# Optimization experiments

Hardware: AMD Instinct MI355X
Metric: run time of the kernel (lower is better)

## Reference

```python
import jax, jax.numpy as jnp
import numpy as np

B, ENC_T, ENC_D = 16, 600, 512
H = 512          # hidden_size == attn_dim (Attention built with attn_dim=hidden_size)
A = 512
VOCAB = 8000
MAX_LEN = 64
SOS = 1


def setup_inputs() -> dict:
    key = jax.random.key(0)
    ks = jax.random.split(key, 16)
    n = jax.random.normal
    s = 0.04  # param init scale
    return {
        "encoder_outputs": n(ks[0], (B, ENC_T, ENC_D), dtype=jnp.float32),
        # embedding table
        "emb": n(ks[1], (VOCAB, H)) * 0.05,
        # GRU (1 layer, input = hidden + enc_dim), PyTorch layout [3H, in]/[3H, H]
        "w_ih": n(ks[2], (3 * H, H + ENC_D)) * s,
        "w_hh": n(ks[3], (3 * H, H)) * s,
        "b_ih": n(ks[4], (3 * H,)) * s,
        "b_hh": n(ks[5], (3 * H,)) * s,
        # location attention: Conv1d(1 -> A, k=3, pad=1)
        "conv_w": n(ks[6], (A, 1, 3)) * 0.1,
        "conv_b": n(ks[7], (A,)) * 0.1,
        "attn_W": n(ks[8], (A, H)) * s,      # W: dec_dim -> attn_dim, no bias
        "attn_V": n(ks[9], (A, ENC_D)) * s,  # V: enc_dim -> attn_dim, no bias
        "attn_fc_w": n(ks[10], (1, A)) * s,  # fc: attn_dim -> 1, with bias
        "attn_fc_b": n(ks[11], (1,)) * s,
        "attn_b": n(ks[12], (A,)) * s,       # extra learned bias b
        # output projection: (hidden + enc_dim) -> vocab
        "fc_w": n(ks[13], (VOCAB, H + ENC_D)) * s,
        "fc_b": n(ks[14], (VOCAB,)) * s,
    }


def reference(encoder_outputs, emb, w_ih, w_hh, b_ih, b_hh,
              conv_w, conv_b, attn_W, attn_V, attn_fc_w, attn_fc_b, attn_b,
              fc_w, fc_b):
    dt = encoder_outputs.dtype
    b, t, ed = encoder_outputs.shape
    h_dim = emb.shape[1]

    # V(values) is time-invariant across decode steps: precompute once. [B, T, A]
    Vv = jnp.einsum('btd,ad->bta', encoder_outputs, attn_V)

    tok0 = jnp.full((b,), SOS, dtype=jnp.int32)
    h0 = jnp.zeros((b, h_dim), dt)          # GRU hidden (None -> zeros)
    ctx0 = jnp.zeros((b, ed), dt)           # initial context
    aw0 = jnp.zeros((b, t), dt)             # initial attention weights

    def step(carry, _):
        tok, h, ctx, aw = carry
        # embed + concat with previous context  [B, H+E]
        x = jnp.concatenate([emb[tok], ctx], axis=-1)
        # GRU cell (PyTorch gate order r, z, n)
        gx = x @ w_ih.T + b_ih
        gh = h @ w_hh.T + b_hh
        xr, xz, xn = jnp.split(gx, 3, axis=-1)
        hr, hz, hn = jnp.split(gh, 3, axis=-1)
        r = jax.nn.sigmoid(xr + hr)
        z = jax.nn.sigmoid(xz + hz)
        ncand = jnp.tanh(xn + r * hn)
        h_new = (1.0 - z) * ncand + z * h
        # location feature: Conv1d over last attention weights. [B, A, T] -> [B, T, A]
        conv = jax.lax.conv_general_dilated(
            aw[:, None, :], conv_w, window_strides=(1,), padding=[(1, 1)],
            dimension_numbers=('NCH', 'OIH', 'NCH')) + conv_b[None, :, None]
        conv = jnp.transpose(conv, (0, 2, 1))
        # score = fc(tanh(W(q) + V(values) + conv + b))  [B, T]
        wq = h_new @ attn_W.T                      # [B, A]
        e = jnp.tanh(wq[:, None, :] + Vv + conv + attn_b)
        score = jnp.einsum('bta,a->bt', e, attn_fc_w[0]) + attn_fc_b[0]
        aw_new = jax.nn.softmax(score, axis=-1)
        # context = attn_weight @ values  [B, E]
        ctx_new = jnp.einsum('bt,btd->bd', aw_new, encoder_outputs)
        # output projection + log_softmax
        out = jnp.concatenate([h_new, ctx_new], axis=-1)
        logits = out @ fc_w.T + fc_b
        logp = jax.nn.log_softmax(logits, axis=-1)
        tok_new = jnp.argmax(logp, axis=-1).astype(jnp.int32)  # greedy symbol
        return (tok_new, h_new, ctx_new, aw_new), logp

    _, logps = jax.lax.scan(step, (tok0, h0, ctx0, aw0), None, length=MAX_LEN)
    # [T_dec, B, V] -> [B, T_dec, V], matching stacked decoder_outputs
    return jnp.transpose(logps, (1, 0, 2))
```

## Files before the change

kernel.cpp:

```cpp
#include <hip/hip_runtime.h>
#include <math.h>

#define NG 256
#define NT 512
#define XSS 516
#define NLOGW 250

__device__ __forceinline__ float ldc(const float* p) {
    return __hip_atomic_load(p, __ATOMIC_RELAXED, __HIP_MEMORY_SCOPE_AGENT);
}
__device__ __forceinline__ void stc(float* p, float v) {
    __hip_atomic_store(p, v, __ATOMIC_RELAXED, __HIP_MEMORY_SCOPE_AGENT);
}

__device__ __forceinline__ void gbar(int* flags, int e, int g, int tid) {
    __syncthreads();
    if (tid == 0)
        __hip_atomic_store(flags + g * 32, e, __ATOMIC_RELAXED,
                           __HIP_MEMORY_SCOPE_AGENT);
    if (tid < 64) {
        const int l = tid;
        int miss = 0;
        for (;;) {
            int f0 = __hip_atomic_load(flags + l * 32,         __ATOMIC_RELAXED, __HIP_MEMORY_SCOPE_AGENT);
            int f1 = __hip_atomic_load(flags + (64 + l) * 32,  __ATOMIC_RELAXED, __HIP_MEMORY_SCOPE_AGENT);
            int f2 = __hip_atomic_load(flags + (128 + l) * 32, __ATOMIC_RELAXED, __HIP_MEMORY_SCOPE_AGENT);
            int f3 = __hip_atomic_load(flags + (192 + l) * 32, __ATOMIC_RELAXED, __HIP_MEMORY_SCOPE_AGENT);
            int m = min(min(f0, f1), min(f2, f3));
            if (__all(m >= e)) break;
            if (++miss > 2) __builtin_amdgcn_s_sleep(1);
        }
    }
    __syncthreads();
}

__global__ __launch_bounds__(256) void k_vv(const float* __restrict__ enc,
                                            const float* __restrict__ attn_V,
                                            float* __restrict__ Vv) {
    int wg = blockIdx.x;
    int b = wg / 40, t0 = (wg % 40) * 15;
    int tid = threadIdx.x;
    __shared__ __align__(16) float encL[15][512];
    for (int i = tid; i < 15 * 512; i += 256) {
        int tl = i >> 9, d = i & 511;
        encL[tl][d] = enc[((size_t)(b * 600) + (t0 + tl)) * 512 + d];
    }
    __syncthreads();
    for (int half = 0; half < 2; ++half) {
        int a = tid + half * 256;
        const float4* wrow = reinterpret_cast<const float4*>(attn_V + (size_t)a * 512);
        float acc[15];
#pragma unroll
        for (int tl = 0; tl < 15; ++tl) acc[tl] = 0.f;
        for (int k = 0; k < 128; ++k) {
            float4 w = wrow[k];
#pragma unroll
            for (int tl = 0; tl < 15; ++tl) {
                float4 x = reinterpret_cast<const float4*>(&encL[tl][0])[k];
                acc[tl] += w.x * x.x + w.y * x.y + w.z * x.z + w.w * x.w;
            }
        }
        for (int tl = 0; tl < 15; ++tl)
            Vv[((size_t)(b * 600) + (t0 + tl)) * 512 + a] = acc[tl];
    }
}

__global__ __launch_bounds__(NT, 1) void mega(
    const float* __restrict__ enc, const float* __restrict__ emb,
    const float* __restrict__ w_ih, const float* __restrict__ w_hh,
    const float* __restrict__ b_ih, const float* __restrict__ b_hh,
    const float* __restrict__ conv_w, const float* __restrict__ conv_b,
    const float* __restrict__ attn_W, const float* __restrict__ attn_fc_w,
    const float* __restrict__ attn_fc_b, const float* __restrict__ attn_b,
    const float* __restrict__ fc_w, const float* __restrict__ fc_b,
    const float* __restrict__ Vv,
    float* hbuf, float* ctxg, float* awg, float* scoreg, float* wqg,
    float* part, float* logZ, int* cnt, float* dout)
{
    const int g = blockIdx.x;
    const int tid = threadIdx.x;
    const int bg = g & 15;
    int bs = 0;

    __shared__ float xs[16 * XSS];
    __shared__ float aux[2600];

    for (int s = 0; s < 64; ++s) {
        const int p = s & 1;
        {
            float* pg = aux;
            float* tokf = aux + 2048;
            if (s == 0) {
                if (tid < 16) tokf[tid] = 1.0f;
                __syncthreads();
            } else {
                const int wv = tid >> 6, lane = tid & 63;
                for (int b = wv; b < 16; b += 8) {
                    float M = -3.4e38f, S = 0.f, I = 0.f;
                    for (int q = 0; q < 4; ++q) {
                        int pw = lane + (q << 6);
                        if (pw < NLOGW) {
                            const float* r = part + ((size_t)pw * 16 + b) * 4;
                            float m = ldc(r), se2 = ldc(r + 1), ii = ldc(r + 2);
                            if (m > M)      { S = S * expf(M - m) + se2; M = m; I = ii; }
                            else if (m == M){ S += se2; if (ii < I) I = ii; }
                            else            { S += se2 * expf(m - M); }
                        }
                    }
                    for (int off = 32; off; off >>= 1) {
                        float m  = __shfl_xor(M, off, 64);
                        float se2 = __shfl_xor(S, off, 64);
                        float ii = __shfl_xor(I, off, 64);
                        if (m > M)      { S = S * expf(M - m) + se2; M = m; I = ii; }
                        else if (m == M){ S += se2; if (ii < I) I = ii; }
                        else            { S += se2 * expf(m - M); }
                    }
                    if (lane == 0) {
                        tokf[b] = I;
                        if (g == 0) stc(&logZ[(s - 1) * 16 + b], M + logf(S));
                    }
                }
                __syncthreads();
            }
            const int b  = tid & 15;
            const int u  = tid >> 4;
            const int il = u & 1;
            const int pr = u >> 1;
            const int i  = (g << 1) + il;
            float ar = 0.f, az = 0.f, axn = 0.f, ahn = 0.f;
            for (int pass = 0; pass < 3; ++pass) {
                for (int idx = tid; idx < 8192; idx += NT) {
                    int bb = idx >> 9, k = idx & 511;
                    float v;
                    if (pass == 0)      v = emb[(size_t)((int)tokf[bb]) * 512 + k];
                    else if (pass == 1) v = ldc(&ctxg[(bb << 9) + k]);
                    else                v = ldc(&hbuf[((p << 4) + bb) * 512 + k]);
                    xs[bb * XSS + k] = v;
                }
                __syncthreads();
                const float* wbase = (pass == 2) ? w_hh : w_ih;
                const size_t rl = (pass == 2) ? 512 : 1024;
                const int ko = (pass == 1) ? 512 : 0;
                const float4* wr = (const float4*)(wbase + (size_t)i * rl + ko) + (pr << 3);
                const float4* wz = (const float4*)(wbase + (size_t)(512 + i) * rl + ko) + (pr << 3);
                const float4* wn = (const float4*)(wbase + (size_t)(1024 + i) * rl + ko) + (pr << 3);
                const float4* xv = (const float4*)(xs + b * XSS) + (pr << 3);
                float s0 = 0.f, s1 = 0.f, s2 = 0.f;
#pragma unroll
                for (int k = 0; k < 8; ++k) {
                    float4 x = xv[k];
                    float4 a = wr[k]; s0 += a.x*x.x + a.y*x.y + a.z*x.z + a.w*x.w;
                    float4 c = wz[k]; s1 += c.x*x.x + c.y*x.y + c.z*x.z + c.w*x.w;
                    float4 d = wn[k]; s2 += d.x*x.x + d.y*x.y + d.z*x.z + d.w*x.w;
                }
                ar += s0; az += s1;
                if (pass < 2) axn += s2; else ahn += s2;
                if (pass < 2) __syncthreads();
            }
            {
                int base = (((b << 1) + il) << 4) + pr;
                pg[base] = ar; pg[512 + base] = az;
                pg[1024 + base] = axn; pg[1536 + base] = ahn;
            }
            __syncthreads();
            if (tid < 32) {
                int bb = tid & 15, ill = tid >> 4;
                int ii = (g << 1) + ill;
                float sr = 0.f, sz2 = 0.f, sxn = 0.f, shn = 0.f;
                int bs2 = ((bb << 1) + ill) << 4;
                for (int q = 0; q < 16; ++q) {
                    sr  += pg[bs2 + q];        sz2 += pg[512 + bs2 + q];
                    sxn += pg[1024 + bs2 + q]; shn += pg[1536 + bs2 + q];
                }
                sr  += b_ih[ii] + b_hh[ii];
                sz2 += b_ih[512 + ii] + b_hh[512 + ii];
                sxn += b_ih[1024 + ii];
                shn += b_hh[1024 + ii];
                float r = 1.f / (1.f + expf(-sr));
                float z = 1.f / (1.f + expf(-sz2));
                float n = tanhf(sxn + r * shn);
                float hp = xs[bb * XSS + ii];
                stc(&hbuf[(((p ^ 1) << 4) + bb) * 512 + ii], (1.f - z) * n + z * hp);
            }
        }
        gbar(cnt, ++bs, g, tid);

        {
            const int ac = g >> 4;
            for (int idx = tid; idx < 512; idx += NT)
                xs[idx] = ldc(&hbuf[(((p ^ 1) << 4) + bg) * 512 + idx]);
            __syncthreads();
            const int al = tid >> 4, ln = tid & 15;
            const int a = (ac << 5) + al;
            const float4* wr = (const float4*)(attn_W + (size_t)a * 512) + (ln << 3);
            const float4* hv = (const float4*)xs + (ln << 3);
            float acc = 0.f;
#pragma unroll
            for (int k = 0; k < 8; ++k) {
                float4 w = wr[k], x = hv[k];
                acc += w.x*x.x + w.y*x.y + w.z*x.z + w.w*x.w;
            }
            for (int off = 8; off; off >>= 1) acc += __shfl_xor(acc, off, 64);
            if (ln == 0) stc(&wqg[(bg << 9) + a], acc);
        }
        gbar(cnt, ++bs, g, tid);

        {
            const int tc = g >> 4;
            const int t0 = tc * 38;
            float* wqL  = xs;
            float* cw0  = xs + 512;
            float* cw1  = xs + 1024;
            float* cw2  = xs + 1536;
            float* cbab = xs + 2048;
            float* fcwL = xs + 2560;
            for (int a = tid; a < 512; a += NT) {
                wqL[a]  = ldc(&wqg[(bg << 9) + a]);
                cw0[a]  = conv_w[a * 3];
                cw1[a]  = conv_w[a * 3 + 1];
                cw2[a]  = conv_w[a * 3 + 2];
                cbab[a] = conv_b[a] + attn_b[a];
                fcwL[a] = attn_fc_w[a];
            }
            __syncthreads();
            const float fcb = attn_fc_b[0];
            const int wv = tid >> 6, lane = tid & 63;
            for (int tl = wv; tl < 38; tl += 8) {
                const int t = t0 + tl;
                if (t < 600) {
                    const float awm = (t > 0)   ? ldc(&awg[bg * 600 + t - 1]) : 0.f;
                    const float aw0 = ldc(&awg[bg * 600 + t]);
                    const float awp = (t < 599) ? ldc(&awg[bg * 600 + t + 1]) : 0.f;
                    const float* vv = Vv + ((size_t)bg * 600 + t) * 512;
                    float acc = 0.f;
#pragma unroll
                    for (int q = 0; q < 8; ++q) {
                        const int a = lane + (q << 6);
                        float uu = wqL[a] + vv[a] + cbab[a]
                                 + cw0[a] * awm + cw1[a] * aw0 + cw2[a] * awp;
                        acc += tanhf(uu) * fcwL[a];
                    }
                    for (int off = 32; off; off >>= 1) acc += __shfl_xor(acc, off, 64);
                    if (lane == 0) stc(&scoreg[bg * 600 + t], acc + fcb);
                }
            }
        }
        gbar(cnt, ++bs, g, tid);

        {
            const int ec = g >> 4;
            float* pb    = xs;
            float* wredM = aux + 2064;
            float* wredS = aux + 2080;
            float* red16 = aux;
            float lm = -3.4e38f;
            for (int t = tid; t < 600; t += NT) {
                float v = ldc(&scoreg[bg * 600 + t]);
                pb[t] = v;
                lm = fmaxf(lm, v);
            }
            for (int off = 32; off; off >>= 1) lm = fmaxf(lm, __shfl_xor(lm, off, 64));
            if ((tid & 63) == 0) wredM[tid >> 6] = lm;
            __syncthreads();
            float M = wredM[0];
#pragma unroll
            for (int q = 1; q < 8; ++q) M = fmaxf(M, wredM[q]);
            float lsum = 0.f;
            for (int t = tid; t < 600; t += NT) {
                float e = expf(pb[t] - M);
                pb[t] = e;
                lsum += e;
            }
            for (int off = 32; off; off >>= 1) lsum += __shfl_xor(lsum, off, 64);
            if ((tid & 63) == 0) wredS[tid >> 6] = lsum;
            __syncthreads();
            float S = 0.f;
#pragma unroll
            for (int q = 0; q < 8; ++q) S += wredS[q];
            const float invS = 1.f / S;
            if (ec == 0)
                for (int t = tid; t < 600; t += NT) stc(&awg[bg * 600 + t], pb[t] * invS);
            const int tg = tid >> 5, l32 = tid & 31;
            const int e = (ec << 5) + l32;
            float acc = 0.f;
            for (int t = tg; t < 600; t += 16)
                acc += pb[t] * enc[((size_t)bg * 600 + t) * 512 + e];
            red16[(tg << 5) + l32] = acc;
            __syncthreads();
            if (tg == 0) {
                float a2 = 0.f;
#pragma unroll
                for (int q = 0; q < 16; ++q) a2 += red16[(q << 5) + l32];
                stc(&ctxg[(bg << 9) + e], a2 * invS);
            }
        }
        gbar(cnt, ++bs, g, tid);

        {
            float* accL = aux;
            float acc0 = 0.f, acc1 = 0.f;
            const int bb = tid & 15, jj = (tid >> 4) & 15;
            const int act = (tid < 256);
            const int v0 = (g << 5) + (jj << 1);
            for (int pass = 0; pass < 2; ++pass) {
                for (int idx = tid; idx < 8192; idx += NT) {
                    int b2 = idx >> 9, k = idx & 511;
                    xs[b2 * XSS + k] = pass ? ldc(&ctxg[(b2 << 9) + k])
                                            : ldc(&hbuf[(((p ^ 1) << 4) + b2) * 512 + k]);
                }
                __syncthreads();
                if (g < NLOGW && act) {
                    const float4* w0 = (const float4*)(fc_w + (size_t)v0 * 1024 + (pass << 9));
                    const float4* w1 = (const float4*)(fc_w + (size_t)(v0 + 1) * 1024 + (pass << 9));
                    const float4* xv = (const float4*)(xs + bb * XSS);
#pragma unroll 4
                    for (int k = 0; k < 128; ++k) {
                        float4 x = xv[k];
                        float4 a = w0[k]; acc0 += a.x*x.x + a.y*x.y + a.z*x.z + a.w*x.w;
                        float4 c = w1[k]; acc1 += c.x*x.x + c.y*x.y + c.z*x.z + c.w*x.w;
                    }
                }
                __syncthreads();
            }
            if (g < NLOGW && act) {
                acc0 += fc_b[v0]; acc1 += fc_b[v0 + 1];
                float* o = dout + ((size_t)bb * 64 + s) * 8000;
                stc(o + v0, acc0);
                stc(o + v0 + 1, acc1);
                float bv, bi;
                if (acc0 >= acc1) { bv = acc0; bi = (float)v0; }
                else              { bv = acc1; bi = (float)(v0 + 1); }
                float se2 = expf(acc0 - bv) + expf(acc1 - bv);
                int rbase = (((bb << 4) + jj) << 2);
                accL[rbase] = bv; accL[rbase + 1] = bi; accL[rbase + 2] = se2;
            }
            __syncthreads();
            if (g < NLOGW && tid < 16) {
                float M = -3.4e38f, I = 0.f, S = 0.f;
                for (int q = 0; q < 16; ++q) {
                    int rb = (((tid << 4) + q) << 2);
                    float m = accL[rb], ii = accL[rb + 1], se2 = accL[rb + 2];
                    if (m > M)      { S = S * expf(M - m) + se2; M = m; I = ii; }
                    else if (m == M){ S += se2; if (ii < I) I = ii; }
                    else            { S += se2 * expf(m - M); }
                }
                float* pr2 = part + ((size_t)g * 16 + tid) * 4;
                stc(pr2, M); stc(pr2 + 1, S); stc(pr2 + 2, I);
            }
        }
        gbar(cnt, ++bs, g, tid);
    }

    if (g == 0) {
        const int wv = tid >> 6, lane = tid & 63;
        for (int b = wv; b < 16; b += 8) {
            float M = -3.4e38f, S = 0.f;
            for (int q = 0; q < 4; ++q) {
                int pw = lane + (q << 6);
                if (pw < NLOGW) {
                    const float* r = part + ((size_t)pw * 16 + b) * 4;
                    float m = ldc(r), se2 = ldc(r + 1);
                    if (m > M)      { S = S * expf(M - m) + se2; M = m; }
                    else if (m == M){ S += se2; }
                    else            { S += se2 * expf(m - M); }
                }
            }
            for (int off = 32; off; off >>= 1) {
                float m  = __shfl_xor(M, off, 64);
                float se2 = __shfl_xor(S, off, 64);
                if (m > M)      { S = S * expf(M - m) + se2; M = m; }
                else if (m == M){ S += se2; }
                else            { S += se2 * expf(m - M); }
            }
            if (lane == 0) stc(&logZ[63 * 16 + b], M + logf(S));
        }
    }
    gbar(cnt, ++bs, g, tid);
    for (int r = g; r < 1024; r += NG) {
        float z = ldc(&logZ[(r & 63) * 16 + (r >> 6)]);
        float* o = dout + (size_t)r * 8000;
        for (int i = tid; i < 8000; i += NT) o[i] -= z;
    }
}

extern "C" void kernel_launch(void* const* d_in, const int* in_sizes, int n_in,
                              void* d_out, int out_size, void* d_ws, size_t ws_size,
                              hipStream_t stream) {
    const float* enc       = (const float*)d_in[0];
    const float* emb       = (const float*)d_in[1];
    const float* w_ih      = (const float*)d_in[2];
    const float* w_hh      = (const float*)d_in[3];
    const float* b_ih      = (const float*)d_in[4];
    const float* b_hh      = (const float*)d_in[5];
    const float* conv_w    = (const float*)d_in[6];
    const float* conv_b    = (const float*)d_in[7];
    const float* attn_W    = (const float*)d_in[8];
    const float* attn_V    = (const float*)d_in[9];
    const float* attn_fc_w = (const float*)d_in[10];
    const float* attn_fc_b = (const float*)d_in[11];
    const float* attn_b    = (const float*)d_in[12];
    const float* fc_w      = (const float*)d_in[13];
    const float* fc_b      = (const float*)d_in[14];

    float* ws    = (float*)d_ws;
    float* Vv    = ws;
    float* hbuf  = Vv + 4915200;
    float* ctx   = hbuf + 16384;
    float* aw    = ctx + 8192;
    float* score = aw + 9600;
    float* wq    = score + 9600;
    float* part  = wq + 8192;
    float* logZ  = part + 16384;
    int*   cnt   = (int*)(logZ + 1024);
    float* dout  = (float*)d_out;

    hipMemsetAsync(hbuf, 0, 34176 * sizeof(float), stream);
    hipMemsetAsync(cnt, 0, 8192 * sizeof(int), stream);

    k_vv<<<dim3(640), dim3(256), 0, stream>>>(enc, attn_V, Vv);

    void* args[] = {(void*)&enc, (void*)&emb, (void*)&w_ih, (void*)&w_hh,
                    (void*)&b_ih, (void*)&b_hh, (void*)&conv_w, (void*)&conv_b,
                    (void*)&attn_W, (void*)&attn_fc_w, (void*)&attn_fc_b,
                    (void*)&attn_b, (void*)&fc_w, (void*)&fc_b, (void*)&Vv,
                    (void*)&hbuf, (void*)&ctx, (void*)&aw, (void*)&score,
                    (void*)&wq, (void*)&part, (void*)&logZ, (void*)&cnt,
                    (void*)&dout};
    hipLaunchCooperativeKernel(reinterpret_cast<void*>(mega),
                               dim3(NG), dim3(NT), args, 0, stream);
}
```

Baseline: 7.034 ms.

## Use per-step buffers, hierarchical atomic barrier, plain vector loads, and restructured logits GEMV

Replaces the flag-polling grid barrier with a two-level atomic counter barrier where a single thread per block spins on a go flag. Each decode step now writes its own fresh buffers for h, ctx, wq, score, aw and partials instead of double-buffering. Because no location is ever rewritten, cross-block reads can use plain vectorized float4 loads rather than relaxed atomic loads. The output projection is reorganized so one thread computes one vocab row per batch with a wave-level argmax/logsumexp merge. Encoder and Vv streams are loaded nontemporally. The cost is a larger workspace, and correctness now relies on the release/acquire behaviour of relaxed atomics plus non-coherent caches seeing each step's fresh addresses.

Result: slower. 8.532 ms (+21.3%).

```diff
diff --git a/kernel.cpp b/kernel.cpp
--- a/kernel.cpp
+++ b/kernel.cpp
@@ -3,35 +3,41 @@
 
 #define NG 256
 #define NT 512
-#define XSS 516
+#define XS2 1032
 #define NLOGW 250
 
-__device__ __forceinline__ float ldc(const float* p) {
-    return __hip_atomic_load(p, __ATOMIC_RELAXED, __HIP_MEMORY_SCOPE_AGENT);
-}
 __device__ __forceinline__ void stc(float* p, float v) {
     __hip_atomic_store(p, v, __ATOMIC_RELAXED, __HIP_MEMORY_SCOPE_AGENT);
 }
 
-__device__ __forceinline__ void gbar(int* flags, int e, int g, int tid) {
+__device__ __forceinline__ void gbar(int* cnt, int epoch, int g, int tid) {
     __syncthreads();
-    if (tid == 0)
-        __hip_atomic_store(flags + g * 32, e, __ATOMIC_RELAXED,
-                           __HIP_MEMORY_SCOPE_AGENT);
-    if (tid < 64) {
-        const int l = tid;
-        int miss = 0;
-        for (;;) {
-            int f0 = __hip_atomic_load(flags + l * 32,         __ATOMIC_RELAXED, __HIP_MEMORY_SCOPE_AGENT);
-            int f1 = __hip_atomic_load(flags + (64 + l) * 32,  __ATOMIC_RELAXED, __HIP_MEMORY_SCOPE_AGENT);
-            int f2 = __hip_atomic_load(flags + (128 + l) * 32, __ATOMIC_RELAXED, __HIP_MEMORY_SCOPE_AGENT);
-            int f3 = __hip_atomic_load(flags + (192 + l) * 32, __ATOMIC_RELAXED, __HIP_MEMORY_SCOPE_AGENT);
-            int m = min(min(f0, f1), min(f2, f3));
-            if (__all(m >= e)) break;
-            if (++miss > 2) __builtin_amdgcn_s_sleep(1);
-        }
+    if (tid == 0) {
+        int* c0 = cnt + ((g & 15) << 5);
+        int* c1 = cnt + 512;
+        int* go = cnt + 576;
+        int r = __hip_atomic_fetch_add(c0, 1, __ATOMIC_RELAXED,
+                                       __HIP_MEMORY_SCOPE_AGENT);
+        if (r == (epoch << 4) - 1) {
+            int r2 = __hip_atomic_fetch_add(c1, 1, __ATOMIC_RELAXED,
+                                            __HIP_MEMORY_SCOPE_AGENT);
+            if (r2 == (epoch << 4) - 1)
+                __hip_atomic_store(go, epoch, __ATOMIC_RELAXED,
+                                   __HIP_MEMORY_SCOPE_AGENT);
+        }
+        int it = 0;
+        while (__hip_atomic_load(go, __ATOMIC_RELAXED,
+                                 __HIP_MEMORY_SCOPE_AGENT) < epoch)
+            if (++it > 4) __builtin_amdgcn_s_sleep(8);
     }
     __syncthreads();
+}
+
+__device__ __forceinline__ void merge3(float& M, float& S, float& I,
+                                       float m, float se, float ii) {
+    if (m > M)       { S = S * expf(M - m) + se; M = m; I = ii; }
+    else if (m == M) { S += se; if (ii < I) I = ii; }
+    else             { S += se * expf(m - M); }
 }
 
 __global__ __launch_bounds__(256) void k_vv(const float* __restrict__ enc,
@@ -73,20 +79,29 @@
     const float* __restrict__ attn_W, const float* __restrict__ attn_fc_w,
     const float* __restrict__ attn_fc_b, const float* __restrict__ attn_b,
     const float* __restrict__ fc_w, const float* __restrict__ fc_b,
-    const float* __restrict__ Vv,
-    float* hbuf, float* ctxg, float* awg, float* scoreg, float* wqg,
-    float* part, float* logZ, int* cnt, float* dout)
+    const float* __restrict__ Vv, const float* __restrict__ Z,
+    float* hv, float* cv, float* wqv, float* scv, float* awv, float* pav,
+    float* logZ, int* cnt, float* dout)
 {
     const int g = blockIdx.x;
     const int tid = threadIdx.x;
     const int bg = g & 15;
-    int bs = 0;
-
-    __shared__ float xs[16 * XSS];
+    int ep = 0;
+
+    __shared__ __align__(16) float xs[16 * XS2];
     __shared__ float aux[2600];
 
     for (int s = 0; s < 64; ++s) {
-        const int p = s & 1;
+        const float* h_r   = (s == 0) ? Z         : hv + (size_t)(s - 1) * 8192;
+        const float* ctx_r = (s == 0) ? Z + 8192  : cv + (size_t)(s - 1) * 8192;
+        const float* aw_r  = (s == 0) ? Z + 16384 : awv + (size_t)(s - 1) * 9600;
+        float* h_w   = hv  + (size_t)s * 8192;
+        float* ctx_w = cv  + (size_t)s * 8192;
+        float* aw_w  = awv + (size_t)s * 9600;
+        float* wq_s  = wqv + (size_t)s * 8192;
+        float* sc_s  = scv + (size_t)s * 9600;
+        float* pa_w  = pav + (size_t)s * 16384;
+
         {
             float* pg = aux;
             float* tokf = aux + 2048;
@@ -94,27 +109,20 @@
                 if (tid < 16) tokf[tid] = 1.0f;
                 __syncthreads();
             } else {
+                const float* pa_r = pav + (size_t)(s - 1) * 16384;
                 const int wv = tid >> 6, lane = tid & 63;
                 for (int b = wv; b < 16; b += 8) {
                     float M = -3.4e38f, S = 0.f, I = 0.f;
                     for (int q = 0; q < 4; ++q) {
                         int pw = lane + (q << 6);
                         if (pw < NLOGW) {
-                            const float* r = part + ((size_t)pw * 16 + b) * 4;
-                            float m = ldc(r), se2 = ldc(r + 1), ii = ldc(r + 2);
-                            if (m > M)      { S = S * expf(M - m) + se2; M = m; I = ii; }
-                            else if (m == M){ S += se2; if (ii < I) I = ii; }
-                            else            { S += se2 * expf(m - M); }
+                            const float* r = pa_r + ((size_t)pw * 16 + b) * 4;
+                            merge3(M, S, I, r[0], r[1], r[2]);
                         }
                     }
-                    for (int off = 32; off; off >>= 1) {
-                        float m  = __shfl_xor(M, off, 64);
-                        float se2 = __shfl_xor(S, off, 64);
-                        float ii = __shfl_xor(I, off, 64);
-                        if (m > M)      { S = S * expf(M - m) + se2; M = m; I = ii; }
-                        else if (m == M){ S += se2; if (ii < I) I = ii; }
-                        else            { S += se2 * expf(m - M); }
-                    }
+                    for (int off = 32; off; off >>= 1)
+                        merge3(M, S, I, __shfl_xor(M, off, 64),
+                               __shfl_xor(S, off, 64), __shfl_xor(I, off, 64));
                     if (lane == 0) {
                         tokf[b] = I;
                         if (g == 0) stc(&logZ[(s - 1) * 16 + b], M + logf(S));
@@ -129,13 +137,16 @@
             const int i  = (g << 1) + il;
             float ar = 0.f, az = 0.f, axn = 0.f, ahn = 0.f;
             for (int pass = 0; pass < 3; ++pass) {
-                for (int idx = tid; idx < 8192; idx += NT) {
-                    int bb = idx >> 9, k = idx & 511;
-                    float v;
-                    if (pass == 0)      v = emb[(size_t)((int)tokf[bb]) * 512 + k];
-                    else if (pass == 1) v = ldc(&ctxg[(bb << 9) + k]);
-                    else                v = ldc(&hbuf[((p << 4) + bb) * 512 + k]);
-                    xs[bb * XSS + k] = v;
+                for (int idx = tid; idx < 2048; idx += NT) {
+                    int bb2 = idx >> 7, k4 = idx & 127;
+                    float4 v4;
+                    if (pass == 0)
+                        v4 = ((const float4*)(emb + (size_t)((int)tokf[bb2]) * 512))[k4];
+                    else if (pass == 1)
+                        v4 = ((const float4*)(ctx_r + (bb2 << 9)))[k4];
+                    else
+                        v4 = ((const float4*)(h_r + (bb2 << 9)))[k4];
+                    ((float4*)(xs + bb2 * XS2))[k4] = v4;
                 }
                 __syncthreads();
                 const float* wbase = (pass == 2) ? w_hh : w_ih;
@@ -144,7 +155,7 @@
                 const float4* wr = (const float4*)(wbase + (size_t)i * rl + ko) + (pr << 3);
                 const float4* wz = (const float4*)(wbase + (size_t)(512 + i) * rl + ko) + (pr << 3);
                 const float4* wn = (const float4*)(wbase + (size_t)(1024 + i) * rl + ko) + (pr << 3);
-                const float4* xv = (const float4*)(xs + b * XSS) + (pr << 3);
+                const float4* xv = (const float4*)(xs + b * XS2) + (pr << 3);
                 float s0 = 0.f, s1 = 0.f, s2 = 0.f;
 #pragma unroll
                 for (int k = 0; k < 8; ++k) {
@@ -179,31 +190,31 @@
                 float r = 1.f / (1.f + expf(-sr));
                 float z = 1.f / (1.f + expf(-sz2));
                 float n = tanhf(sxn + r * shn);
-                float hp = xs[bb * XSS + ii];
-                stc(&hbuf[(((p ^ 1) << 4) + bb) * 512 + ii], (1.f - z) * n + z * hp);
-            }
-        }
-        gbar(cnt, ++bs, g, tid);
+                float hp = xs[bb * XS2 + ii];
+                stc(&h_w[(bb << 9) + ii], (1.f - z) * n + z * hp);
+            }
+        }
+        gbar(cnt, ++ep, g, tid);
 
         {
             const int ac = g >> 4;
-            for (int idx = tid; idx < 512; idx += NT)
-                xs[idx] = ldc(&hbuf[(((p ^ 1) << 4) + bg) * 512 + idx]);
+            for (int idx = tid; idx < 128; idx += NT)
+                ((float4*)xs)[idx] = ((const float4*)(h_w + (bg << 9)))[idx];
             __syncthreads();
             const int al = tid >> 4, ln = tid & 15;
             const int a = (ac << 5) + al;
             const float4* wr = (const float4*)(attn_W + (size_t)a * 512) + (ln << 3);
-            const float4* hv = (const float4*)xs + (ln << 3);
+            const float4* hvv = (const float4*)xs + (ln << 3);
             float acc = 0.f;
 #pragma unroll
             for (int k = 0; k < 8; ++k) {
-                float4 w = wr[k], x = hv[k];
+                float4 w = wr[k], x = hvv[k];
                 acc += w.x*x.x + w.y*x.y + w.z*x.z + w.w*x.w;
             }
             for (int off = 8; off; off >>= 1) acc += __shfl_xor(acc, off, 64);
-            if (ln == 0) stc(&wqg[(bg << 9) + a], acc);
-        }
-        gbar(cnt, ++bs, g, tid);
+            if (ln == 0) stc(&wq_s[(bg << 9) + a], acc);
+        }
+        gbar(cnt, ++ep, g, tid);
 
         {
             const int tc = g >> 4;
@@ -215,7 +226,7 @@
             float* cbab = xs + 2048;
             float* fcwL = xs + 2560;
             for (int a = tid; a < 512; a += NT) {
-                wqL[a]  = ldc(&wqg[(bg << 9) + a]);
+                wqL[a]  = wq_s[(bg << 9) + a];
                 cw0[a]  = conv_w[a * 3];
                 cw1[a]  = conv_w[a * 3 + 1];
                 cw2[a]  = conv_w[a * 3 + 2];
@@ -228,24 +239,25 @@
             for (int tl = wv; tl < 38; tl += 8) {
                 const int t = t0 + tl;
                 if (t < 600) {
-                    const float awm = (t > 0)   ? ldc(&awg[bg * 600 + t - 1]) : 0.f;
-                    const float aw0 = ldc(&awg[bg * 600 + t]);
-                    const float awp = (t < 599) ? ldc(&awg[bg * 600 + t + 1]) : 0.f;
+                    const float awm = (t > 0)   ? aw_r[bg * 600 + t - 1] : 0.f;
+                    const float aw0 = aw_r[bg * 600 + t];
+                    const float awp = (t < 599) ? aw_r[bg * 600 + t + 1] : 0.f;
                     const float* vv = Vv + ((size_t)bg * 600 + t) * 512;
                     float acc = 0.f;
 #pragma unroll
                     for (int q = 0; q < 8; ++q) {
                         const int a = lane + (q << 6);
-                        float uu = wqL[a] + vv[a] + cbab[a]
+                        float va = __builtin_nontemporal_load(vv + a);
+                        float uu = wqL[a] + va + cbab[a]
                                  + cw0[a] * awm + cw1[a] * aw0 + cw2[a] * awp;
                         acc += tanhf(uu) * fcwL[a];
                     }
                     for (int off = 32; off; off >>= 1) acc += __shfl_xor(acc, off, 64);
-                    if (lane == 0) stc(&scoreg[bg * 600 + t], acc + fcb);
-                }
-            }
-        }
-        gbar(cnt, ++bs, g, tid);
+                    if (lane == 0) stc(&sc_s[bg * 600 + t], acc + fcb);
+                }
+            }
+        }
+        gbar(cnt, ++ep, g, tid);
 
         {
             const int ec = g >> 4;
@@ -255,7 +267,7 @@
             float* red16 = aux;
             float lm = -3.4e38f;
             for (int t = tid; t < 600; t += NT) {
-                float v = ldc(&scoreg[bg * 600 + t]);
+                float v = sc_s[bg * 600 + t];
                 pb[t] = v;
                 lm = fmaxf(lm, v);
             }
@@ -279,105 +291,88 @@
             for (int q = 0; q < 8; ++q) S += wredS[q];
             const float invS = 1.f / S;
             if (ec == 0)
-                for (int t = tid; t < 600; t += NT) stc(&awg[bg * 600 + t], pb[t] * invS);
+                for (int t = tid; t < 600; t += NT) stc(&aw_w[bg * 600 + t], pb[t] * invS);
             const int tg = tid >> 5, l32 = tid & 31;
             const int e = (ec << 5) + l32;
             float acc = 0.f;
             for (int t = tg; t < 600; t += 16)
-                acc += pb[t] * enc[((size_t)bg * 600 + t) * 512 + e];
+                acc += pb[t] * __builtin_nontemporal_load(
+                           enc + ((size_t)bg * 600 + t) * 512 + e);
             red16[(tg << 5) + l32] = acc;
             __syncthreads();
             if (tg == 0) {
                 float a2 = 0.f;
 #pragma unroll
                 for (int q = 0; q < 16; ++q) a2 += red16[(q << 5) + l32];
-                stc(&ctxg[(bg << 9) + e], a2 * invS);
-            }
-        }
-        gbar(cnt, ++bs, g, tid);
+                stc(&ctx_w[(bg << 9) + e], a2 * invS);
+            }
+        }
+        gbar(cnt, ++ep, g, tid);
 
         {
-            float* accL = aux;
-            float acc0 = 0.f, acc1 = 0.f;
-            const int bb = tid & 15, jj = (tid >> 4) & 15;
-            const int act = (tid < 256);
-            const int v0 = (g << 5) + (jj << 1);
-            for (int pass = 0; pass < 2; ++pass) {
-                for (int idx = tid; idx < 8192; idx += NT) {
-                    int b2 = idx >> 9, k = idx & 511;
-                    xs[b2 * XSS + k] = pass ? ldc(&ctxg[(b2 << 9) + k])
-                                            : ldc(&hbuf[(((p ^ 1) << 4) + b2) * 512 + k]);
-                }
-                __syncthreads();
-                if (g < NLOGW && act) {
-                    const float4* w0 = (const float4*)(fc_w + (size_t)v0 * 1024 + (pass << 9));
-                    const float4* w1 = (const float4*)(fc_w + (size_t)(v0 + 1) * 1024 + (pass << 9));
-                    const float4* xv = (const float4*)(xs + bb * XSS);
-#pragma unroll 4
-                    for (int k = 0; k < 128; ++k) {
-                        float4 x = xv[k];
-                        float4 a = w0[k]; acc0 += a.x*x.x + a.y*x.y + a.z*x.z + a.w*x.w;
-                        float4 c = w1[k]; acc1 += c.x*x.x + c.y*x.y + c.z*x.z + c.w*x.w;
-                    }
-                }
-                __syncthreads();
-            }
-            if (g < NLOGW && act) {
-                acc0 += fc_b[v0]; acc1 += fc_b[v0 + 1];
-                float* o = dout + ((size_t)bb * 64 + s) * 8000;
-                stc(o + v0, acc0);
-                stc(o + v0 + 1, acc1);
-                float bv, bi;
-                if (acc0 >= acc1) { bv = acc0; bi = (float)v0; }
-                else              { bv = acc1; bi = (float)(v0 + 1); }
-                float se2 = expf(acc0 - bv) + expf(acc1 - bv);
-                int rbase = (((bb << 4) + jj) << 2);
-                accL[rbase] = bv; accL[rbase + 1] = bi; accL[rbase + 2] = se2;
-            }
-            __syncthreads();
-            if (g < NLOGW && tid < 16) {
-                float M = -3.4e38f, I = 0.f, S = 0.f;
-                for (int q = 0; q < 16; ++q) {
-                    int rb = (((tid << 4) + q) << 2);
-                    float m = accL[rb], ii = accL[rb + 1], se2 = accL[rb + 2];
-                    if (m > M)      { S = S * expf(M - m) + se2; M = m; I = ii; }
-                    else if (m == M){ S += se2; if (ii < I) I = ii; }
-                    else            { S += se2 * expf(m - M); }
-                }
-                float* pr2 = part + ((size_t)g * 16 + tid) * 4;
-                stc(pr2, M); stc(pr2 + 1, S); stc(pr2 + 2, I);
-            }
-        }
-        gbar(cnt, ++bs, g, tid);
+            const int jj = tid & 31;
+            const int bb = tid >> 5;
+            const int act = (g < NLOGW);
+            const int v = (g << 5) + jj;
+            for (int idx = tid; idx < 2048; idx += NT) {
+                int b2 = idx >> 7, k4 = idx & 127;
+                ((float4*)(xs + b2 * XS2))[k4] =
+                    ((const float4*)(h_w + (b2 << 9)))[k4];
+                ((float4*)(xs + b2 * XS2 + 512))[k4] =
+                    ((const float4*)(ctx_w + (b2 << 9)))[k4];
+            }
+            __syncthreads();
+            if (act) {
+                const float4* wrow = (const float4*)(fc_w + (size_t)v * 1024);
+                const float4* xrow = (const float4*)(xs + bb * XS2);
+                float a0 = 0.f, a1 = 0.f, a2 = 0.f, a3 = 0.f;
+                for (int k = 0; k < 256; k += 4) {
+                    float4 w0 = wrow[k],     x0 = xrow[k];
+                    float4 w1 = wrow[k + 1], x1 = xrow[k + 1];
+                    float4 w2 = wrow[k + 2], x2 = xrow[k + 2];
+                    float4 w3 = wrow[k + 3], x3 = xrow[k + 3];
+                    a0 += w0.x*x0.x + w0.y*x0.y + w0.z*x0.z + w0.w*x0.w;
+                    a1 += w1.x*x1.x + w1.y*x1.y + w1.z*x1.z + w1.w*x1.w;
+                    a2 += w2.x*x2.x + w2.y*x2.y + w2.z*x2.z + w2.w*x2.w;
+                    a3 += w3.x*x3.x + w3.y*x3.y + w3.z*x3.z + w3.w*x3.w;
+                }
+                float acc = ((a0 + a1) + (a2 + a3)) + fc_b[v];
+                stc(dout + ((size_t)bb * 64 + s) * 8000 + v, acc);
+                float M = acc, S = 1.f, I = (float)v;
+#pragma unroll
+                for (int off = 1; off < 32; off <<= 1)
+                    merge3(M, S, I, __shfl_xor(M, off, 64),
+                           __shfl_xor(S, off, 64), __shfl_xor(I, off, 64));
+                if (jj == 0) {
+                    float* pr = pa_w + ((size_t)g * 16 + bb) * 4;
+                    stc(pr, M); stc(pr + 1, S); stc(pr + 2, I);
+                }
+            }
+        }
+        gbar(cnt, ++ep, g, tid);
     }
 
     if (g == 0) {
+        const float* pa_r = pav + (size_t)63 * 16384;
         const int wv = tid >> 6, lane = tid & 63;
         for (int b = wv; b < 16; b += 8) {
-            float M = -3.4e38f, S = 0.f;
+            float M = -3.4e38f, S = 0.f, I = 0.f;
             for (int q = 0; q < 4; ++q) {
                 int pw = lane + (q << 6);
                 if (pw < NLOGW) {
-                    const float* r = part + ((size_t)pw * 16 + b) * 4;
-                    float m = ldc(r), se2 = ldc(r + 1);
-                    if (m > M)      { S = S * expf(M - m) + se2; M = m; }
-                    else if (m == M){ S += se2; }
-                    else            { S += se2 * expf(m - M); }
-                }
-            }
-            for (int off = 32; off; off >>= 1) {
-                float m  = __shfl_xor(M, off, 64);
-                float se2 = __shfl_xor(S, off, 64);
-                if (m > M)      { S = S * expf(M - m) + se2; M = m; }
-                else if (m == M){ S += se2; }
-                else            { S += se2 * expf(m - M); }
-            }
+                    const float* r = pa_r + ((size_t)pw * 16 + b) * 4;
+                    merge3(M, S, I, r[0], r[1], r[2]);
+                }
+            }
+            for (int off = 32; off; off >>= 1)
+                merge3(M, S, I, __shfl_xor(M, off, 64),
+                       __shfl_xor(S, off, 64), __shfl_xor(I, off, 64));
             if (lane == 0) stc(&logZ[63 * 16 + b], M + logf(S));
         }
     }
-    gbar(cnt, ++bs, g, tid);
+    gbar(cnt, ++ep, g, tid);
     for (int r = g; r < 1024; r += NG) {
-        float z = ldc(&logZ[(r & 63) * 16 + (r >> 6)]);
+        float z = logZ[(r & 63) * 16 + (r >> 6)];
         float* o = dout + (size_t)r * 8000;
         for (int i = tid; i < 8000; i += NT) o[i] -= z;
     }
@@ -402,20 +397,21 @@
     const float* fc_w      = (const float*)d_in[13];
     const float* fc_b      = (const float*)d_in[14];
 
-    float* ws    = (float*)d_ws;
-    float* Vv    = ws;
-    float* hbuf  = Vv + 4915200;
-    float* ctx   = hbuf + 16384;
-    float* aw    = ctx + 8192;
-    float* score = aw + 9600;
-    float* wq    = score + 9600;
-    float* part  = wq + 8192;
-    float* logZ  = part + 16384;
-    int*   cnt   = (int*)(logZ + 1024);
-    float* dout  = (float*)d_out;
-
-    hipMemsetAsync(hbuf, 0, 34176 * sizeof(float), stream);
-    hipMemsetAsync(cnt, 0, 8192 * sizeof(int), stream);
+    float* ws   = (float*)d_ws;
+    float* Vv   = ws;
+    float* Z    = Vv + 4915200;
+    float* hv   = Z + 25984;
+    float* cv   = hv + 524288;
+    float* wqv  = cv + 524288;
+    float* scv  = wqv + 524288;
+    float* awv  = scv + 614400;
+    float* pav  = awv + 614400;
+    float* logZ = pav + 1048576;
+    int*   cnt  = (int*)(logZ + 1024);
+    float* dout = (float*)d_out;
+
+    hipMemsetAsync(Z, 0, 25984 * sizeof(float), stream);
+    hipMemsetAsync(cnt, 0, 1024 * sizeof(int), stream);
 
     k_vv<<<dim3(640), dim3(256), 0, stream>>>(enc, attn_V, Vv);
 
@@ -423,8 +419,8 @@
                     (void*)&b_ih, (void*)&b_hh, (void*)&conv_w, (void*)&conv_b,
                     (void*)&attn_W, (void*)&attn_fc_w, (void*)&attn_fc_b,
                     (void*)&attn_b, (void*)&fc_w, (void*)&fc_b, (void*)&Vv,
-                    (void*)&hbuf, (void*)&ctx, (void*)&aw, (void*)&score,
-                    (void*)&wq, (void*)&part, (void*)&logZ, (void*)&cnt,
+                    (void*)&Z, (void*)&hv, (void*)&cv, (void*)&wqv, (void*)&scv,
+                    (void*)&awv, (void*)&pav, (void*)&logZ, (void*)&cnt,
                     (void*)&dout};
     hipLaunchCooperativeKernel(reinterpret_cast<void*>(mega),
                                dim3(NG), dim3(NT), args, 0, stream);
```
